# Kernel tuning notes

Hardware: AMD Instinct MI355X
Metric: run time of the kernel (lower is better)

Reference implementation:

```python
import jax, jax.numpy as jnp
import numpy as np

B, T, E, H, C = 256, 512, 512, 1024, 128
DECAY = 0.9  # args.decay_rate


def setup_inputs() -> dict:
    key = jax.random.key(0)
    ks = jax.random.split(key, 9)
    x = jax.random.normal(ks[0], (B, T, E), jnp.float32)
    cate = jax.random.normal(ks[1], (B, T, C), jnp.float32)
    # pack() requires lengths sorted in decreasing order
    seq_lens = jnp.sort(jax.random.randint(ks[2], (B,), T // 2, T + 1))[::-1]
    s = 1.0 / np.sqrt(H)
    W_ih = jax.random.uniform(ks[3], (4 * H, E), jnp.float32, -s, s)
    W_hh = jax.random.uniform(ks[4], (4 * H, H), jnp.float32, -s, s)
    b_ih = jax.random.uniform(ks[5], (4 * H,), jnp.float32, -s, s)
    b_hh = jax.random.uniform(ks[6], (4 * H,), jnp.float32, -s, s)
    s2 = 1.0 / np.sqrt(H + C)
    W_lin = jax.random.uniform(ks[7], (E, H + C), jnp.float32, -s2, s2)
    b_lin = jax.random.uniform(ks[8], (E,), jnp.float32, -s2, s2)
    return dict(x=x, cate=cate, seq_lens=seq_lens, W_ih=W_ih, W_hh=W_hh,
                b_ih=b_ih, b_hh=b_hh, W_lin=W_lin, b_lin=b_lin)


def reference(x, cate, seq_lens, W_ih, W_hh, b_ih, b_hh, W_lin, b_lin):
    # x: [B,T,E], cate: [B,T,C], seq_lens: [B] sorted descending.
    # Packed per-timestep LSTMCell with category EMA blend, expressed as a
    # masked full-batch scan (rows beyond their length never re-activate,
    # so masking outputs is exactly equivalent to the packed slicing).
    Bd, Td, Ed = x.shape
    Hd = W_hh.shape[1]
    Cd = cate.shape[2]

    xs = (jnp.swapaxes(x, 0, 1), jnp.swapaxes(cate, 0, 1), jnp.arange(Td))

    def step(carry, inp):
        h, c, prev_cate = carry
        x_t, cate_t, t = inp
        # EMA blend only for step > 0 (torch: prev_cate*decay + cate*(1-decay))
        cate_eff = jnp.where(t > 0, DECAY * prev_cate + (1.0 - DECAY) * cate_t, cate_t)
        gates = x_t @ W_ih.T + b_ih + h @ W_hh.T + b_hh  # [B,4H]
        i, f, g, o = jnp.split(gates, 4, axis=-1)
        i = jax.nn.sigmoid(i)
        f = jax.nn.sigmoid(f)
        g = jnp.tanh(g)
        o = jax.nn.sigmoid(o)
        c = f * c + i * g
        h = o * jnp.tanh(c)
        active = (t < seq_lens)[:, None]  # [B,1]
        out = jnp.where(active, jnp.concatenate([h, cate_eff], axis=-1), 0.0)
        return (h, c, cate_eff), out

    h0 = jnp.zeros((Bd, Hd), x.dtype)
    c0 = jnp.zeros((Bd, Hd), x.dtype)
    p0 = jnp.zeros((Bd, Cd), x.dtype)
    _, outs = jax.lax.scan(step, (h0, c0, p0), xs)  # [T,B,H+C]
    outs = jnp.swapaxes(outs, 0, 1)  # [B,T,H+C]
    # Linear is applied to padded zeros too (matches torch: linear after fill)
    return outs @ W_lin.T + b_lin  # [B,T,E]
```

## Files before the change

kernel.cpp:

```cpp
#include <hip/hip_runtime.h>
#include <math.h>

#define Bsz 256
#define Tn  512
#define En  512
#define Hn  1024
#define Cn  128
#define DECAY 0.9f

typedef unsigned short u16;
typedef unsigned int   u32;
typedef __attribute__((ext_vector_type(8))) short bf16x8;
typedef __attribute__((ext_vector_type(4))) float f32x4;

__device__ __forceinline__ u16 f2bf(float f) {
  union { float f; u32 u; } v; v.f = f;
  u32 x = v.u;
  return (u16)((x + 0x7fffu + ((x >> 16) & 1u)) >> 16);
}


__global__ void k_prep_wc(const float* __restrict__ Wih, const float* __restrict__ Whh,
                          u16* __restrict__ Wc) {
  int r = blockIdx.x;
  const float* sih = Wih + (size_t)r * En;
  const float* shh = Whh + (size_t)r * Hn;
  u16* dst = Wc + (size_t)r * (En + Hn);
  for (int k = threadIdx.x; k < En + Hn; k += 256) {
    float v = (k < En) ? sih[k] : shh[k - En];
    dst[k] = f2bf(v);
  }
}

__global__ void k_prep_wl(const float* __restrict__ Wlin, u16* __restrict__ Wl) {
  int e = blockIdx.x;
  for (int k = threadIdx.x; k < Hn + Cn; k += 256)
    Wl[(size_t)e * (Hn + Cn) + k] = f2bf(Wlin[(size_t)e * (Hn + Cn) + k]);
}

__global__ void k_prep_misc(const float* __restrict__ bih, const float* __restrict__ bhh,
                            const int* __restrict__ seq,
                            float* __restrict__ biasg, int* __restrict__ nb,
                            float* __restrict__ cst, u16* __restrict__ hbuf) {
  const int total = 4096 + 512 + Bsz * Hn + 2 * Bsz * Hn;
  for (int i = blockIdx.x * 256 + threadIdx.x; i < total; i += gridDim.x * 256) {
    if (i < 4096) {
      biasg[i] = bih[i] + bhh[i];
    } else if (i < 4608) {
      int t = i - 4096, cnt = 0;
      for (int b = 0; b < Bsz; ++b) cnt += (seq[b] > t) ? 1 : 0;
      nb[t] = cnt;
    } else if (i < 4608 + Bsz * Hn) {
      cst[i - 4608] = 0.f;
    } else {
      hbuf[i - (4608 + Bsz * Hn)] = 0;
    }
  }
}

__global__ void k_ema(const float* __restrict__ cate, u16* __restrict__ ce) {
  int b = blockIdx.x;
  int ch = threadIdx.x;
  float prev = 0.f;
  for (int t = 0; t < Tn; ++t) {
    float v = cate[((size_t)b * Tn + t) * Cn + ch];
    float eff = (t == 0) ? v : (DECAY * prev + (1.f - DECAY) * v);
    prev = eff;
    ce[((size_t)b * Tn + t) * Cn + ch] = f2bf(eff);
  }
}

__global__ void k_prefill(float* __restrict__ out, const float* __restrict__ blin) {
  size_t i = (size_t)blockIdx.x * 256 + threadIdx.x;
  int e = (int)((i * 4) & (En - 1));
  *(float4*)(out + i * 4) = *(const float4*)(blin + e);
}

__global__ __launch_bounds__(256)
void k_step(int t,
            const float* __restrict__ x, const int* __restrict__ nb,
            const u16* __restrict__ Wc, const float* __restrict__ biasg,
            const u16* __restrict__ Wl, const float* __restrict__ blin,
            const u16* __restrict__ ce,
            float* __restrict__ cst, u16* __restrict__ hbuf,
            float* __restrict__ out) {
  __shared__ __align__(16) u16 As[32 * 40];
  __shared__ __align__(16) u16 Bs[4 * 32 * 40];
  __shared__ float gbuf[4 * 32 * 32];

  const int tid  = threadIdx.x;
  const int wave = tid >> 6, lane = tid & 63;
  const int nrow  = lane & 15;
  const int khalf = lane >> 4;
  const int kcol  = khalf * 8;

  const int ar = tid >> 3;
  const int ak = (tid & 7) * 4;
  const int bn = lane >> 1;
  const int bh = (lane & 1) * 16;

  if (blockIdx.x < 256) {
    if (t >= Tn) return;
    const int nbt = nb[t];
    const int bm = blockIdx.x >> 5, hn = blockIdx.x & 31;
    const int b0 = bm * 32, j0 = hn * 32;
    if (b0 >= nbt) return;

    const u16* __restrict__ hprev = hbuf + (size_t)(t & 1) * (Bsz * Hn);
    u16* __restrict__ hnext = hbuf + (size_t)((t + 1) & 1) * (Bsz * Hn);

    f32x4 acc[2][2] = {};
    const u16* wrow = Wc + (size_t)(wave * Hn + j0 + bn) * 1536;

    for (int kc = 0; kc < 48; ++kc) {
      const int k0 = kc * 32;
      {
        const int k = k0 + ak;
        const int b = b0 + ar;
        if (k < En) {
          const float4 v = *(const float4*)(x + ((size_t)b * Tn + t) * En + k);
          ushort4 s;
          s.x = f2bf(v.x); s.y = f2bf(v.y); s.z = f2bf(v.z); s.w = f2bf(v.w);
          *(ushort4*)(As + ar * 40 + ak) = s;
        } else {
          *(ushort4*)(As + ar * 40 + ak) =
              *(const ushort4*)(hprev + (size_t)b * Hn + (k - En));
        }
      }
      {
        const u16* p = wrow + k0 + bh;
        uint4 v0 = *(const uint4*)p;
        uint4 v1 = *(const uint4*)(p + 8);
        u16* q = Bs + (wave * 32 + bn) * 40 + bh;
        *(uint4*)q = v0;
        *(uint4*)(q + 8) = v1;
      }
      __syncthreads();
      bf16x8 a0  = *(const bf16x8*)(As + nrow * 40 + kcol);
      bf16x8 a1  = *(const bf16x8*)(As + (16 + nrow) * 40 + kcol);
      bf16x8 bb0 = *(const bf16x8*)(Bs + (wave * 32 + nrow) * 40 + kcol);
      bf16x8 bb1 = *(const bf16x8*)(Bs + (wave * 32 + 16 + nrow) * 40 + kcol);
      acc[0][0] = __builtin_amdgcn_mfma_f32_16x16x32_bf16(a0, bb0, acc[0][0], 0, 0, 0);
      acc[0][1] = __builtin_amdgcn_mfma_f32_16x16x32_bf16(a0, bb1, acc[0][1], 0, 0, 0);
      acc[1][0] = __builtin_amdgcn_mfma_f32_16x16x32_bf16(a1, bb0, acc[1][0], 0, 0, 0);
      acc[1][1] = __builtin_amdgcn_mfma_f32_16x16x32_bf16(a1, bb1, acc[1][1], 0, 0, 0);
      __syncthreads();
    }

    for (int mi = 0; mi < 2; ++mi)
      for (int ni = 0; ni < 2; ++ni) {
        const int n = ni * 16 + nrow;
        const float bg = biasg[wave * Hn + j0 + n];
        for (int r = 0; r < 4; ++r) {
          const int m = mi * 16 + khalf * 4 + r;
          gbuf[wave * 1024 + m * 32 + n] = acc[mi][ni][r] + bg;
        }
      }
    __syncthreads();

    for (int p = tid; p < 1024; p += 256) {
      const int m = p >> 5, n = p & 31;
      const int b = b0 + m, j = j0 + n;
      const float gi = gbuf[0 * 1024 + p];
      const float gf = gbuf[1 * 1024 + p];
      const float gg = gbuf[2 * 1024 + p];
      const float go = gbuf[3 * 1024 + p];
      const float si = 1.f / (1.f + __expf(-gi));
      const float sf = 1.f / (1.f + __expf(-gf));
      const float tg = tanhf(gg);
      const float so = 1.f / (1.f + __expf(-go));
      const size_t idx = (size_t)b * Hn + j;
      const float cn = sf * cst[idx] + si * tg;
      cst[idx] = cn;
      hnext[idx] = f2bf(so * tanhf(cn));
    }
  } else {
    if (t == 0) return;
    const int tl = t - 1;
    const int nbl = nb[tl];
    const int lid = blockIdx.x - 256;
    const int bm = lid >> 2, en = lid & 3;
    const int b0 = bm * 32, e0 = en * 128;
    if (b0 >= nbl) return;

    const u16* __restrict__ hcur = hbuf + (size_t)(t & 1) * (Bsz * Hn);

    f32x4 acc[2][2] = {};
    const u16* wrow = Wl + (size_t)(e0 + wave * 32 + bn) * 1152;

    for (int kc = 0; kc < 36; ++kc) {
      const int k0 = kc * 32;
      {
        const int k = k0 + ak;
        const int b = b0 + ar;
        const u16* src = (k < Hn)
            ? (hcur + (size_t)b * Hn + k)
            : (ce + ((size_t)b * Tn + tl) * Cn + (k - Hn));
        *(ushort4*)(As + ar * 40 + ak) = *(const ushort4*)src;
      }
      {
        const u16* p = wrow + k0 + bh;
        uint4 v0 = *(const uint4*)p;
        uint4 v1 = *(const uint4*)(p + 8);
        u16* q = Bs + (wave * 32 + bn) * 40 + bh;
        *(uint4*)q = v0;
        *(uint4*)(q + 8) = v1;
      }
      __syncthreads();
      bf16x8 a0  = *(const bf16x8*)(As + nrow * 40 + kcol);
      bf16x8 a1  = *(const bf16x8*)(As + (16 + nrow) * 40 + kcol);
      bf16x8 bb0 = *(const bf16x8*)(Bs + (wave * 32 + nrow) * 40 + kcol);
      bf16x8 bb1 = *(const bf16x8*)(Bs + (wave * 32 + 16 + nrow) * 40 + kcol);
      acc[0][0] = __builtin_amdgcn_mfma_f32_16x16x32_bf16(a0, bb0, acc[0][0], 0, 0, 0);
      acc[0][1] = __builtin_amdgcn_mfma_f32_16x16x32_bf16(a0, bb1, acc[0][1], 0, 0, 0);
      acc[1][0] = __builtin_amdgcn_mfma_f32_16x16x32_bf16(a1, bb0, acc[1][0], 0, 0, 0);
      acc[1][1] = __builtin_amdgcn_mfma_f32_16x16x32_bf16(a1, bb1, acc[1][1], 0, 0, 0);
      __syncthreads();
    }

    for (int mi = 0; mi < 2; ++mi)
      for (int ni = 0; ni < 2; ++ni) {
        const int e = e0 + wave * 32 + ni * 16 + nrow;
        const float bl = blin[e];
        for (int r = 0; r < 4; ++r) {
          const int b = b0 + mi * 16 + khalf * 4 + r;
          if (b < nbl)
            out[((size_t)b * Tn + tl) * En + e] = acc[mi][ni][r] + bl;
        }
      }
  }
}

extern "C" void kernel_launch(void* const* d_in, const int* in_sizes, int n_in,
                              void* d_out, int out_size, void* d_ws, size_t ws_size,
                              hipStream_t stream) {
  const float* x    = (const float*)d_in[0];
  const float* cate = (const float*)d_in[1];
  const int*   seq  = (const int*)d_in[2];
  const float* Wih  = (const float*)d_in[3];
  const float* Whh  = (const float*)d_in[4];
  const float* bih  = (const float*)d_in[5];
  const float* bhh  = (const float*)d_in[6];
  const float* Wlin = (const float*)d_in[7];
  const float* blin = (const float*)d_in[8];
  float* out = (float*)d_out;

  char* w = (char*)d_ws;
  u16*   Wc    = (u16*)w;   w += (size_t)4096 * 1536 * 2;
  u16*   Wl    = (u16*)w;   w += (size_t)512 * 1152 * 2;
  float* biasg = (float*)w; w += (size_t)4096 * 4;
  int*   nb    = (int*)w;   w += (size_t)512 * 4;
  u16*   ce    = (u16*)w;   w += (size_t)Bsz * Tn * Cn * 2;
  float* cst   = (float*)w; w += (size_t)Bsz * Hn * 4;
  u16*   hb    = (u16*)w;   w += (size_t)2 * Bsz * Hn * 2;
  (void)ws_size; (void)in_sizes; (void)n_in; (void)out_size;

  k_prep_wc<<<4096, 256, 0, stream>>>(Wih, Whh, Wc);
  k_prep_wl<<<512, 256, 0, stream>>>(Wlin, Wl);
  k_prep_misc<<<3090, 256, 0, stream>>>(bih, bhh, seq, biasg, nb, cst, hb);
  k_ema<<<256, 128, 0, stream>>>(cate, ce);
  k_prefill<<<65536, 256, 0, stream>>>(out, blin);

  for (int t = 0; t <= Tn; ++t)
    k_step<<<288, 256, 0, stream>>>(t, x, nb, Wc, biasg, Wl, blin, ce, cst, hb, out);
}
```

Baseline: 17.05 ms.

## Replace per-timestep launches with persistent cooperative kernel holding weights in registers

Replaces the 513 per-timestep kernel launches with a single cooperative persistent kernel of 256 blocks that uses a software grid barrier between the recurrent gate GEMM and the output projection. Each block keeps its slice of the gate-interleaved combined weight matrix in registers and its slice of the linear weights in LDS. The cell state also stays in registers, and the next timestep's x tile is prefetched and double-buffered. This targets launch overhead and repeated weight reloads from memory. In exchange it depends on all 256 blocks being co-resident, spin-waits on atomics every step, and still runs the prep for the old weight layout.

```diff
diff --git a/kernel.cpp b/kernel.cpp
--- a/kernel.cpp
+++ b/kernel.cpp
@@ -1,4 +1,5 @@
 #include <hip/hip_runtime.h>
+#include <hip/hip_bf16.h>
 #include <math.h>
 
 #define Bsz 256
@@ -17,6 +18,13 @@
   union { float f; u32 u; } v; v.f = f;
   u32 x = v.u;
   return (u16)((x + 0x7fffu + ((x >> 16) & 1u)) >> 16);
+}
+
+__device__ __forceinline__ u32 pk2(float a, float b) {
+  float2 f2; f2.x = a; f2.y = b;
+  __hip_bfloat162 h = __float22bfloat162_rn(f2);
+  union { __hip_bfloat162 h; u32 u; } v; v.h = h;
+  return v.u;
 }
 
 
@@ -32,6 +40,18 @@
   }
 }
 
+__global__ void k_prep_wp(const float* __restrict__ Wih, const float* __restrict__ Whh,
+                          u16* __restrict__ Wp) {
+  int p = blockIdx.x;
+  int jt = p >> 5, n = p & 31, g = n >> 3, jj = n & 7;
+  int orig = g * 1024 + jt * 8 + jj;
+  u16* dst = Wp + (size_t)p * 1536;
+  for (int k = threadIdx.x; k < 1536; k += 256) {
+    float v = (k < En) ? Wih[(size_t)orig * En + k] : Whh[(size_t)orig * Hn + (k - En)];
+    dst[k] = f2bf(v);
+  }
+}
+
 __global__ void k_prep_wl(const float* __restrict__ Wlin, u16* __restrict__ Wl) {
   int e = blockIdx.x;
   for (int k = threadIdx.x; k < Hn + Cn; k += 256)
@@ -40,21 +60,27 @@
 
 __global__ void k_prep_misc(const float* __restrict__ bih, const float* __restrict__ bhh,
                             const int* __restrict__ seq,
-                            float* __restrict__ biasg, int* __restrict__ nb,
-                            float* __restrict__ cst, u16* __restrict__ hbuf) {
-  const int total = 4096 + 512 + Bsz * Hn + 2 * Bsz * Hn;
+                            float* __restrict__ biasg, float* __restrict__ bgp,
+                            int* __restrict__ nb, float* __restrict__ cst,
+                            u16* __restrict__ hbuf, int* __restrict__ bar) {
+  const int total = 4096 + 4096 + 512 + 2 + Bsz * Hn + 2 * Bsz * Hn;
   for (int i = blockIdx.x * 256 + threadIdx.x; i < total; i += gridDim.x * 256) {
-    if (i < 4096) {
-      biasg[i] = bih[i] + bhh[i];
-    } else if (i < 4608) {
-      int t = i - 4096, cnt = 0;
-      for (int b = 0; b < Bsz; ++b) cnt += (seq[b] > t) ? 1 : 0;
-      nb[t] = cnt;
-    } else if (i < 4608 + Bsz * Hn) {
-      cst[i - 4608] = 0.f;
-    } else {
-      hbuf[i - (4608 + Bsz * Hn)] = 0;
-    }
+    int j = i;
+    if (j < 4096) { biasg[j] = bih[j] + bhh[j]; continue; }
+    j -= 4096;
+    if (j < 4096) {
+      int g = (j & 31) >> 3, jj = j & 7, jt = j >> 5;
+      int orig = g * 1024 + jt * 8 + jj;
+      bgp[j] = bih[orig] + bhh[orig]; continue;
+    }
+    j -= 4096;
+    if (j < 512) { int cnt = 0; for (int b = 0; b < Bsz; ++b) cnt += (seq[b] > j) ? 1 : 0; nb[j] = cnt; continue; }
+    j -= 512;
+    if (j < 2) { bar[j] = 0; continue; }
+    j -= 2;
+    if (j < Bsz * Hn) { cst[j] = 0.f; continue; }
+    j -= Bsz * Hn;
+    hbuf[j] = 0;
   }
 }
 
@@ -93,7 +119,6 @@
   const int nrow  = lane & 15;
   const int khalf = lane >> 4;
   const int kcol  = khalf * 8;
-
   const int ar = tid >> 3;
   const int ak = (tid & 7) * 4;
   const int bn = lane >> 1;
@@ -231,6 +256,223 @@
   }
 }
 
+#define SMEM_BYTES 129792
+
+__device__ __forceinline__ void gridbar(int* __restrict__ bar) {
+  __syncthreads();
+  if (threadIdx.x == 0) {
+    int g = __hip_atomic_load(bar + 1, __ATOMIC_RELAXED, __HIP_MEMORY_SCOPE_AGENT);
+    if (__hip_atomic_fetch_add(bar, 1, __ATOMIC_ACQ_REL, __HIP_MEMORY_SCOPE_AGENT) == 255) {
+      __hip_atomic_store(bar, 0, __ATOMIC_RELAXED, __HIP_MEMORY_SCOPE_AGENT);
+      __hip_atomic_fetch_add(bar + 1, 1, __ATOMIC_RELEASE, __HIP_MEMORY_SCOPE_AGENT);
+    } else {
+      while (__hip_atomic_load(bar + 1, __ATOMIC_ACQUIRE, __HIP_MEMORY_SCOPE_AGENT) == g)
+        __builtin_amdgcn_s_sleep(1);
+    }
+  }
+  __syncthreads();
+}
+
+__device__ __forceinline__ void load_f4x8(const float* __restrict__ src, float4* r) {
+#pragma unroll
+  for (int j = 0; j < 8; ++j) r[j] = *(const float4*)(src + j * 4);
+}
+
+__device__ __forceinline__ void pack_write(u16* __restrict__ dst, const float4* r) {
+#pragma unroll
+  for (int j2 = 0; j2 < 4; ++j2) {
+    union { u32 u[4]; bf16x8 v; } p;
+    p.u[0] = pk2(r[2 * j2].x,     r[2 * j2].y);
+    p.u[1] = pk2(r[2 * j2].z,     r[2 * j2].w);
+    p.u[2] = pk2(r[2 * j2 + 1].x, r[2 * j2 + 1].y);
+    p.u[3] = pk2(r[2 * j2 + 1].z, r[2 * j2 + 1].w);
+    *(bf16x8*)(dst + j2 * 8) = p.v;
+  }
+}
+
+__global__ __launch_bounds__(256, 1)
+void k_persist(const float* __restrict__ x, const int* __restrict__ nb,
+               const u16* __restrict__ Wp, const float* __restrict__ bgp,
+               const u16* __restrict__ Wl, const float* __restrict__ blin,
+               const u16* __restrict__ ce, u16* __restrict__ hb,
+               float* __restrict__ out, int* __restrict__ bar) {
+  extern __shared__ char smem[];
+  u16*   WlL  = (u16*)(smem);
+  u16*   gA   = (u16*)(smem + 74240);
+  u16*   lA   = (u16*)(smem + 111104);
+  float* gbuf = (float*)(smem + 111104);
+  float* pacc = (float*)(smem + 111104);
+
+  const int tid  = threadIdx.x, blk = blockIdx.x;
+  const int wave = tid >> 6, lane = tid & 63;
+  const int nrow = lane & 15, kh = lane >> 4;
+  const int wm = wave >> 1, wn = wave & 1;
+  const int bm = blk >> 7, jt = blk & 127;
+  const int b0 = bm * 128;
+  const int rt = blk >> 4, ct = blk & 15;
+  const int r0 = rt * 16, e0 = ct * 32;
+  const int srow = tid & 127, sseg = tid >> 7;
+  const int crow = tid >> 1, jj0 = (tid & 1) * 4;
+
+  for (int i = tid; i < 4608; i += 256) {
+    const int row = i & 31, g = i >> 5;
+    *(bf16x8*)(WlL + row * 1160 + g * 8) =
+        *(const bf16x8*)(Wl + (size_t)(e0 + row) * 1152 + g * 8);
+  }
+
+  bf16x8 wf[48];
+  {
+    const u16* wp = Wp + (size_t)(jt * 32 + wn * 16 + nrow) * 1536 + kh * 8;
+#pragma unroll
+    for (int c = 0; c < 48; ++c) wf[c] = *(const bf16x8*)(wp + c * 32);
+  }
+  const float bias_r = bgp[jt * 32 + wn * 16 + nrow];
+  float creg[4] = {0.f, 0.f, 0.f, 0.f};
+
+  float4 xr[8], xr2[8];
+  bf16x8 hr[4];
+
+  {
+    const float* s0 = x + (size_t)(b0 + srow) * (Tn * En) + sseg * 32;
+    load_f4x8(s0, xr2);
+    load_f4x8(s0 + 64, xr);
+    pack_write(gA + srow * 72 + sseg * 32, xr2);
+  }
+  __syncthreads();
+
+  for (int t = 0; t < Tn; ++t) {
+    const int nbt = nb[t];
+    const int nbn = (t < Tn - 1) ? nb[t + 1] : 0;
+
+    if (b0 < nbt) {
+      const u16* __restrict__ hprev = hb + (size_t)((t + 1) & 1) * (Bsz * Hn);
+      f32x4 acc[4] = {};
+#pragma unroll
+      for (int kc = 0; kc < 24; ++kc) {
+        if (kc >= 1 && kc < 23) {
+          if (kc + 1 < 8) {
+            const float* src = x + ((size_t)(b0 + srow) * Tn + t) * En + (kc + 1) * 64 + sseg * 32;
+            load_f4x8(src, xr);
+          } else {
+            const u16* src = hprev + (size_t)(b0 + srow) * Hn + (kc + 1 - 8) * 64 + sseg * 32;
+#pragma unroll
+            for (int j = 0; j < 4; ++j) hr[j] = *(const bf16x8*)(src + j * 8);
+          }
+        }
+        {
+          const u16* base = gA + (kc & 1) * 9216;
+#pragma unroll
+          for (int s = 0; s < 2; ++s) {
+#pragma unroll
+            for (int mf = 0; mf < 4; ++mf) {
+              bf16x8 a = *(const bf16x8*)(base + (wm * 64 + mf * 16 + nrow) * 72 + s * 32 + kh * 8);
+              acc[mf] = __builtin_amdgcn_mfma_f32_16x16x32_bf16(a, wf[2 * kc + s], acc[mf], 0, 0, 0);
+            }
+          }
+        }
+        if (kc < 23) {
+          u16* dst = gA + ((kc + 1) & 1) * 9216 + srow * 72 + sseg * 32;
+          if (kc + 1 < 8) {
+            pack_write(dst, xr);
+          } else {
+#pragma unroll
+            for (int j = 0; j < 4; ++j) *(bf16x8*)(dst + j * 8) = hr[j];
+          }
+        }
+        __syncthreads();
+      }
+
+#pragma unroll
+      for (int mf = 0; mf < 4; ++mf)
+#pragma unroll
+        for (int r = 0; r < 4; ++r)
+          gbuf[(wm * 64 + mf * 16 + kh * 4 + r) * 34 + wn * 16 + nrow] = acc[mf][r] + bias_r;
+      __syncthreads();
+
+      {
+        const int b = b0 + crow;
+        if (b < nbt) {
+          const float* gr = gbuf + crow * 34 + jj0;
+          ushort4 hv;
+          u16 hvv[4];
+#pragma unroll
+          for (int r = 0; r < 4; ++r) {
+            const float gi = gr[r], gf = gr[8 + r], gg = gr[16 + r], go = gr[24 + r];
+            const float si = 1.f / (1.f + __expf(-gi));
+            const float sf = 1.f / (1.f + __expf(-gf));
+            const float tg = tanhf(gg);
+            const float so = 1.f / (1.f + __expf(-go));
+            const float cn = sf * creg[r] + si * tg;
+            creg[r] = cn;
+            hvv[r] = f2bf(so * tanhf(cn));
+          }
+          hv.x = hvv[0]; hv.y = hvv[1]; hv.z = hvv[2]; hv.w = hvv[3];
+          *(ushort4*)(hb + (size_t)(t & 1) * (Bsz * Hn) + (size_t)b * Hn + jt * 8 + jj0) = hv;
+        }
+      }
+
+      if (t < Tn - 1 && b0 < nbn) {
+        const float* s0 = x + ((size_t)(b0 + srow) * Tn + (t + 1)) * En + sseg * 32;
+        load_f4x8(s0, xr2);
+        load_f4x8(s0 + 64, xr);
+        pack_write(gA + srow * 72 + sseg * 32, xr2);
+      }
+    }
+
+    gridbar(bar);
+
+    if (r0 < nbt) {
+      f32x4 lacc[2] = {};
+      const u16* __restrict__ hcur = hb + (size_t)(t & 1) * (Bsz * Hn);
+#pragma unroll
+      for (int half = 0; half < 2; ++half) {
+        for (int i = tid; i < 1152; i += 256) {
+          const int row = i & 15, g = i >> 4;
+          const int k = half * 576 + g * 8;
+          const u16* src = (k < Hn)
+              ? (hcur + (size_t)(r0 + row) * Hn + k)
+              : (ce + ((size_t)(r0 + row) * Tn + t) * Cn + (k - Hn));
+          *(bf16x8*)(lA + row * 584 + g * 8) = *(const bf16x8*)src;
+        }
+        __syncthreads();
+#pragma unroll
+        for (int c9 = 0; c9 < 9; ++c9) {
+          const int c = half * 9 + c9;
+          if ((c & 3) == wave) {
+#pragma unroll
+            for (int s = 0; s < 2; ++s) {
+              bf16x8 a = *(const bf16x8*)(lA + nrow * 584 + c9 * 64 + s * 32 + kh * 8);
+#pragma unroll
+              for (int nf = 0; nf < 2; ++nf) {
+                bf16x8 b = *(const bf16x8*)(WlL + (nf * 16 + nrow) * 1160 + c * 64 + s * 32 + kh * 8);
+                lacc[nf] = __builtin_amdgcn_mfma_f32_16x16x32_bf16(a, b, lacc[nf], 0, 0, 0);
+              }
+            }
+          }
+        }
+        __syncthreads();
+      }
+#pragma unroll
+      for (int nf = 0; nf < 2; ++nf)
+#pragma unroll
+        for (int r = 0; r < 4; ++r)
+          pacc[wave * 528 + (kh * 4 + r) * 33 + nf * 16 + nrow] = lacc[nf][r];
+      __syncthreads();
+#pragma unroll
+      for (int ii = 0; ii < 2; ++ii) {
+        const int idx = tid * 2 + ii;
+        const int m = idx >> 5, n = idx & 31;
+        if (r0 + m < nbt) {
+          float v = pacc[m * 33 + n] + pacc[528 + m * 33 + n]
+                  + pacc[1056 + m * 33 + n] + pacc[1584 + m * 33 + n]
+                  + blin[e0 + n];
+          out[((size_t)(r0 + m) * Tn + t) * En + e0 + n] = v;
+        }
+      }
+    }
+  }
+}
+
 extern "C" void kernel_launch(void* const* d_in, const int* in_sizes, int n_in,
                               void* d_out, int out_size, void* d_ws, size_t ws_size,
                               hipStream_t stream) {
@@ -247,20 +489,37 @@
 
   char* w = (char*)d_ws;
   u16*   Wc    = (u16*)w;   w += (size_t)4096 * 1536 * 2;
+  u16*   Wp    = (u16*)w;   w += (size_t)4096 * 1536 * 2;
   u16*   Wl    = (u16*)w;   w += (size_t)512 * 1152 * 2;
   float* biasg = (float*)w; w += (size_t)4096 * 4;
+  float* bgp   = (float*)w; w += (size_t)4096 * 4;
   int*   nb    = (int*)w;   w += (size_t)512 * 4;
+  int*   bar   = (int*)w;   w += (size_t)64;
   u16*   ce    = (u16*)w;   w += (size_t)Bsz * Tn * Cn * 2;
   float* cst   = (float*)w; w += (size_t)Bsz * Hn * 4;
   u16*   hb    = (u16*)w;   w += (size_t)2 * Bsz * Hn * 2;
   (void)ws_size; (void)in_sizes; (void)n_in; (void)out_size;
 
   k_prep_wc<<<4096, 256, 0, stream>>>(Wih, Whh, Wc);
+  k_prep_wp<<<4096, 256, 0, stream>>>(Wih, Whh, Wp);
   k_prep_wl<<<512, 256, 0, stream>>>(Wlin, Wl);
-  k_prep_misc<<<3090, 256, 0, stream>>>(bih, bhh, seq, biasg, nb, cst, hb);
+  k_prep_misc<<<3107, 256, 0, stream>>>(bih, bhh, seq, biasg, bgp, nb, cst, hb, bar);
   k_ema<<<256, 128, 0, stream>>>(cate, ce);
   k_prefill<<<65536, 256, 0, stream>>>(out, blin);
 
-  for (int t = 0; t <= Tn; ++t)
-    k_step<<<288, 256, 0, stream>>>(t, x, nb, Wc, biasg, Wl, blin, ce, cst, hb, out);
-}
+  static int attr_done = 0;
+  if (!attr_done) {
+    (void)hipFuncSetAttribute((const void*)k_persist,
+                              hipFuncAttributeMaxDynamicSharedMemorySize, SMEM_BYTES);
+    attr_done = 1;
+  }
+
+  void* kargs[] = {(void*)&x, (void*)&nb, (void*)&Wp, (void*)&bgp, (void*)&Wl,
+                   (void*)&blin, (void*)&ce, (void*)&hb, (void*)&out, (void*)&bar};
+  hipError_t err = hipLaunchCooperativeKernel((const void*)k_persist, dim3(256), dim3(256),
+                                              kargs, (unsigned int)SMEM_BYTES, stream);
+  if (err != hipSuccess) {
+    for (int t = 0; t <= Tn; ++t)
+      k_step<<<288, 256, 0, stream>>>(t, x, nb, Wc, biasg, Wl, blin, ce, cst, hb, out);
+  }
+}
```

Result: slower. 40.81 ms (+139.4%).
